# Performance work log

Measured on AMD Instinct MI355X. Metric: run time of the kernel, lower is better.

The kernel has to match this reference:

```python
import jax, jax.numpy as jnp
import numpy as np

TOP_K = 2

def setup_inputs() -> dict:
    key = jax.random.key(0)
    ks = jax.random.split(key, 8)
    B, T, C, E, I, S = 1, 2048, 2048, 8, 1408, 2816
    s = 0.02  # weight scale for numerical stability
    return {
        "x": jax.random.normal(ks[0], (B, T, C), jnp.float32),
        "gate_w": jax.random.normal(ks[1], (E, C), jnp.float32) * s,
        "w1": jax.random.normal(ks[2], (E, I, C), jnp.float32) * s,
        "w3": jax.random.normal(ks[3], (E, I, C), jnp.float32) * s,
        "w2": jax.random.normal(ks[4], (E, C, I), jnp.float32) * s,
        "sw1": jax.random.normal(ks[5], (S, C), jnp.float32) * s,
        "sw3": jax.random.normal(ks[6], (S, C), jnp.float32) * s,
        "sw2": jax.random.normal(ks[7], (C, S), jnp.float32) * s,
    }

def reference(x, gate_w, w1, w3, w2, sw1, sw3, sw2):
    B, T, C = x.shape
    E = gate_w.shape[0]
    xf = x.reshape(-1, C)                      # [N, C]
    N = xf.shape[0]
    # --- routing: top-k of raw logits, softmax over the k selected logits ---
    logits = xf @ gate_w.T                     # [N, E]
    pv, idx = jax.lax.top_k(logits, TOP_K)     # [N, K]
    pv = jax.nn.softmax(pv.astype(jnp.float32), axis=-1).astype(x.dtype)
    # token-expert combine weights (sum of probs per expert, scatter of top-k)
    tew = jnp.zeros((N, E), x.dtype).at[jnp.arange(N)[:, None], idx].add(pv)
    # --- experts (SwiGLU), computed densely over all experts and masked by tew ---
    h = jax.nn.silu(jnp.einsum('nc,eic->nei', xf, w1)) * jnp.einsum('nc,eic->nei', xf, w3)
    eo = jnp.einsum('nei,eci->nec', h, w2)     # [N, E, C]
    y = jnp.einsum('nec,ne->nc', eo, tew).reshape(B, T, C)
    # --- shared expert on the residual input ---
    sh = (jax.nn.silu(x @ sw1.T) * (x @ sw3.T)) @ sw2.T
    return y + sh
```

## Files before the change

kernel.cpp:

```cpp
#include <hip/hip_runtime.h>

#define DEVI __device__ __forceinline__

typedef __attribute__((ext_vector_type(4))) float f32x4;
typedef __attribute__((ext_vector_type(8))) short bf16x8;

static constexpr int NT = 2048;
static constexpr int CD = 2048;
static constexpr int NE = 8;
static constexpr int ID = 1408;
static constexpr int SD = 2816;
static constexpr int ROWS = 2 * NT;
static constexpr int ROWS_PAD = ROWS + 256;

DEVI unsigned short f2bf(float f) {
  unsigned u = __builtin_bit_cast(unsigned, f);
  u += 0x7fff + ((u >> 16) & 1);
  return (unsigned short)(u >> 16);
}
DEVI float bf2f(unsigned short s) { return __builtin_bit_cast(float, (unsigned)s << 16); }
DEVI float silu_f(float z) { return z / (1.f + __expf(-z)); }

DEVI void gll16(const void* g, void* l) {
  __builtin_amdgcn_global_load_lds((__attribute__((address_space(1))) void*)(void*)g,
                                   (__attribute__((address_space(3))) void*)l, 16, 0, 0);
}

DEVI void bar_sched() {
  __builtin_amdgcn_s_barrier();
  __builtin_amdgcn_sched_barrier(0);
}
DEVI void sched0() { __builtin_amdgcn_sched_barrier(0); }
DEVI void wait_vm0() { asm volatile("s_waitcnt vmcnt(0)" ::: "memory"); }
DEVI void wait_lgk0() { asm volatile("s_waitcnt lgkmcnt(0)" ::: "memory"); }

DEVI int swz8(int bid, int nwg) {
  constexpr int CH = 8, G = 64;
  int nfull = nwg - (nwg % G);
  if (bid >= nfull) return bid;
  int c = bid / G, r = bid % G;
  return c * G + (r % 8) * CH + (r / 8);
}

__global__ __launch_bounds__(256) void k_cvt(const float* __restrict__ s,
                                             unsigned short* __restrict__ d, int n8)
{
  int i = blockIdx.x * 256 + threadIdx.x;
  int stride = gridDim.x * 256;
  for (; i < n8; i += stride) {
    float4 a = ((const float4*)s)[2 * i];
    float4 b = ((const float4*)s)[2 * i + 1];
    ushort4 p0 = make_ushort4(f2bf(a.x), f2bf(a.y), f2bf(a.z), f2bf(a.w));
    ushort4 p1 = make_ushort4(f2bf(b.x), f2bf(b.y), f2bf(b.z), f2bf(b.w));
    ((ushort4*)d)[2 * i]     = p0;
    ((ushort4*)d)[2 * i + 1] = p1;
  }
}

__global__ __launch_bounds__(64) void k_router(const float* __restrict__ x,
    const float* __restrict__ gw, int* __restrict__ counts,
    int* __restrict__ eidx, int* __restrict__ posn, float* __restrict__ probs)
{
  const int n = blockIdx.x;
  const int lane = threadIdx.x;
  const float4* xr = (const float4*)(x + (size_t)n * CD);
  float acc[NE];
#pragma unroll
  for (int e = 0; e < NE; ++e) acc[e] = 0.f;
  for (int i = lane; i < CD / 4; i += 64) {
    float4 xv = xr[i];
#pragma unroll
    for (int e = 0; e < NE; ++e) {
      float4 gv = ((const float4*)(gw + (size_t)e * CD))[i];
      acc[e] += xv.x * gv.x + xv.y * gv.y + xv.z * gv.z + xv.w * gv.w;
    }
  }
#pragma unroll
  for (int e = 0; e < NE; ++e) {
    float v = acc[e];
#pragma unroll
    for (int off = 32; off > 0; off >>= 1) v += __shfl_down(v, off);
    acc[e] = v;
  }
  if (lane == 0) {
    int b0 = 0; float m0 = acc[0];
#pragma unroll
    for (int e = 1; e < NE; ++e) if (acc[e] > m0) { m0 = acc[e]; b0 = e; }
    int b1 = -1; float m1 = 0.f;
#pragma unroll
    for (int e = 0; e < NE; ++e) {
      if (e == b0) continue;
      if (b1 < 0 || acc[e] > m1) { m1 = acc[e]; b1 = e; }
    }
    float d = __expf(m1 - m0);
    float inv = 1.f / (1.f + d);
    eidx[2 * n] = b0; eidx[2 * n + 1] = b1;
    probs[2 * n] = inv; probs[2 * n + 1] = d * inv;
    posn[2 * n] = atomicAdd(&counts[b0], 1);
    posn[2 * n + 1] = atomicAdd(&counts[b1], 1);
  }
}

__global__ void k_scan(const int* __restrict__ counts, int* __restrict__ bases) {
  if (threadIdx.x == 0) {
    int s = 0;
    for (int e = 0; e < NE; ++e) { bases[e] = s; s += counts[e]; }
  }
}

__global__ __launch_bounds__(256) void k_build(const int* __restrict__ eidx,
    const int* __restrict__ posn, const int* __restrict__ bases,
    int* __restrict__ rows_of, int* __restrict__ row2tok)
{
  int n = blockIdx.x * 256 + threadIdx.x;
  if (n >= NT) return;
#pragma unroll
  for (int k = 0; k < 2; ++k) {
    int e = eidx[2 * n + k];
    int row = bases[e] + posn[2 * n + k];
    rows_of[2 * n + k] = row;
    row2tok[row] = n;
  }
}

__global__ __launch_bounds__(512, 2) void k_up(
    const unsigned short* __restrict__ xb,
    const unsigned short* __restrict__ w1b, const unsigned short* __restrict__ w3b,
    const unsigned short* __restrict__ sw1b, const unsigned short* __restrict__ sw3b,
    unsigned short* __restrict__ h, unsigned short* __restrict__ hs,
    const int* __restrict__ counts, const int* __restrict__ bases,
    const int* __restrict__ row2tok)
{
  extern __shared__ char sm[];
  constexpr int NSH = (NT / 256) * (SD / 128);
  constexpr int NWG = NSH + NE * (ID / 128) * (NT / 256);
  constexpr int NSTEP = CD / 64;

  int lin = swz8((int)blockIdx.x, NWG);
  int cls, mx, pn, e = 0;
  if (lin < NSH) { cls = 0; mx = lin % 8; pn = lin / 8; }
  else { cls = 1; int r = lin - NSH; mx = r % 8; r /= 8; pn = r % 11; e = r / 11; }

  int M = NT, baserow = 0;
  if (cls) { M = counts[e]; if (mx * 256 >= M) return; baserow = bases[e]; }
  const int m0 = mx * 256, n0 = pn * 128;

  const unsigned short* B1 = cls ? w1b + ((size_t)e * ID + n0) * CD : sw1b + (size_t)n0 * CD;
  const unsigned short* B3 = cls ? w3b + ((size_t)e * ID + n0) * CD : sw3b + (size_t)n0 * CD;

  const int tid = threadIdx.x, l = tid & 63, w = tid >> 6;
  const int wr = w >> 2, wn = w & 3;
  const int slot = ((tid & 7) ^ ((tid >> 3) & 7)) * 16;

  const char* aP[4];
#pragma unroll
  for (int t = 0; t < 4; ++t) {
    int r = t * 64 + (tid >> 3);
    const unsigned short* rb;
    if (cls) {
      int grow = m0 + r; int gr = grow < M ? grow : 0;
      rb = xb + (size_t)row2tok[baserow + gr] * CD;
    } else {
      rb = xb + (size_t)(m0 + r) * CD;
    }
    aP[t] = (const char*)rb + slot;
  }
  const char* bP1[2]; const char* bP3[2];
#pragma unroll
  for (int t = 0; t < 2; ++t) {
    int r = t * 64 + (tid >> 3);
    bP1[t] = (const char*)(B1 + (size_t)r * CD) + slot;
    bP3[t] = (const char*)(B3 + (size_t)r * CD) + slot;
  }

  f32x4 acc1[8][2], acc3[8][2];
#pragma unroll
  for (int m = 0; m < 8; ++m)
#pragma unroll
    for (int n = 0; n < 2; ++n) {
      acc1[m][n] = {0.f, 0.f, 0.f, 0.f};
      acc3[m][n] = {0.f, 0.f, 0.f, 0.f};
    }

  const int lrow = l & 15, lkg = l >> 4, l7 = l & 7;

  auto stage_first = [&](char* base, size_t kb) {
#pragma unroll
    for (int t = 0; t < 4; ++t) gll16(aP[t] + kb, base + t * 8192 + tid * 16);
  };
  auto stage_second = [&](char* base, size_t kb) {
    char* sB1 = base + 32768; char* sB3 = base + 49152;
#pragma unroll
    for (int t = 0; t < 2; ++t) {
      gll16(bP1[t] + kb, sB1 + t * 8192 + tid * 16);
      gll16(bP3[t] + kb, sB3 + t * 8192 + tid * 16);
    }
  };
  auto ldq = [&](bf16x8* fa, bf16x8* fb1, bf16x8* fb3, const char* cur, int mh, int kk) {
    const char* sA = cur; const char* sB1 = cur + 32768; const char* sB3 = cur + 49152;
    const int ao = ((kk * 4 + lkg) ^ l7) * 16;
#pragma unroll
    for (int m = 0; m < 4; ++m)
      fa[m] = *(const bf16x8*)(sA + (wr * 128 + mh * 64 + m * 16 + lrow) * 128 + ao);
#pragma unroll
    for (int n = 0; n < 2; ++n) {
      fb1[n] = *(const bf16x8*)(sB1 + (wn * 32 + n * 16 + lrow) * 128 + ao);
      fb3[n] = *(const bf16x8*)(sB3 + (wn * 32 + n * 16 + lrow) * 128 + ao);
    }
  };
  auto mmq = [&](const bf16x8* fa, const bf16x8* fb1, const bf16x8* fb3, int mh) {
    __builtin_amdgcn_s_setprio(1);
#pragma unroll
    for (int n = 0; n < 2; ++n)
#pragma unroll
      for (int m = 0; m < 4; ++m) {
        acc1[mh * 4 + m][n] = __builtin_amdgcn_mfma_f32_16x16x32_bf16(fa[m], fb1[n], acc1[mh * 4 + m][n], 0, 0, 0);
        acc3[mh * 4 + m][n] = __builtin_amdgcn_mfma_f32_16x16x32_bf16(fa[m], fb3[n], acc3[mh * 4 + m][n], 0, 0, 0);
      }
    __builtin_amdgcn_s_setprio(0);
  };

  stage_first(sm, 0);
  stage_second(sm, 0);
  wait_vm0(); bar_sched();

  bf16x8 Xa[4], Xb1[2], Xb3[2], Ya[4], Yb1[2], Yb3[2];

  for (int t = 0; t < NSTEP; ++t) {
    char* cur = sm + (size_t)(t & 1) * 65536;
    char* nxt = sm + (size_t)((t + 1) & 1) * 65536;
    size_t kb = (size_t)(t + 1) * 128;
    ldq(Xa, Xb1, Xb3, cur, 0, 0);
    sched0();
    if (t + 1 < NSTEP) stage_first(nxt, kb);
    ldq(Ya, Yb1, Yb3, cur, 1, 0);
    mmq(Xa, Xb1, Xb3, 0);
    sched0();
    if (t + 1 < NSTEP) stage_second(nxt, kb);
    ldq(Xa, Xb1, Xb3, cur, 0, 1);
    mmq(Ya, Yb1, Yb3, 1);
    sched0();
    ldq(Ya, Yb1, Yb3, cur, 1, 1);
    mmq(Xa, Xb1, Xb3, 0);
    sched0();
    mmq(Ya, Yb1, Yb3, 1);
    sched0();
    wait_vm0(); wait_lgk0();
    bar_sched();
  }

#pragma unroll
  for (int m = 0; m < 8; ++m) {
    int rb_ = m0 + wr * 128 + m * 16 + lkg * 4;
#pragma unroll
    for (int j = 0; j < 4; ++j) {
      int grow = rb_ + j;
      if (cls && grow >= M) continue;
#pragma unroll
      for (int n = 0; n < 2; ++n) {
        int gcol = n0 + wn * 32 + n * 16 + lrow;
        float hh = silu_f(acc1[m][n][j]) * acc3[m][n][j];
        if (cls) h[(size_t)(baserow + grow) * ID + gcol] = f2bf(hh);
        else     hs[(size_t)grow * SD + gcol] = f2bf(hh);
      }
    }
  }
}

__global__ __launch_bounds__(512, 2) void k_down(
    const unsigned short* __restrict__ h, const unsigned short* __restrict__ hs,
    const unsigned short* __restrict__ w2b, const unsigned short* __restrict__ sw2b,
    unsigned short* __restrict__ eo, float* __restrict__ y,
    const int* __restrict__ counts, const int* __restrict__ bases)
{
  extern __shared__ char sm[];
  constexpr int NRT = NE * (CD / 256) * (NT / 256);
  constexpr int NWG = NRT + (CD / 256) * (NT / 256);

  int lin = swz8((int)blockIdx.x, NWG);
  int cls, mx, pn, e = 0;
  if (lin < NRT) { cls = 1; mx = lin % 8; int r = lin / 8; pn = r % 8; e = r / 8; }
  else { cls = 0; int r = lin - NRT; mx = r % 8; pn = r / 8; }

  int M = NT, baserow = 0;
  if (cls) { M = counts[e]; if (mx * 256 >= M) return; baserow = bases[e]; }
  const int m0 = mx * 256, n0 = pn * 256;
  const int KD_ = cls ? ID : SD;
  const int nstep = KD_ / 64;

  const unsigned short* B = cls ? w2b + ((size_t)e * CD + n0) * ID : sw2b + (size_t)n0 * SD;

  const int tid = threadIdx.x, l = tid & 63, w = tid >> 6;
  const int wr = w >> 2, wn = w & 3;
  const int slot = ((tid & 7) ^ ((tid >> 3) & 7)) * 16;

  const char* aP[4]; const char* bP[4];
#pragma unroll
  for (int t = 0; t < 4; ++t) {
    int r = t * 64 + (tid >> 3);
    const unsigned short* rb = cls ? h + (size_t)(baserow + m0 + r) * ID
                                   : hs + (size_t)(m0 + r) * SD;
    aP[t] = (const char*)rb + slot;
    bP[t] = (const char*)(B + (size_t)r * KD_) + slot;
  }

  f32x4 acc[8][4];
#pragma unroll
  for (int m = 0; m < 8; ++m)
#pragma unroll
    for (int n = 0; n < 4; ++n) acc[m][n] = {0.f, 0.f, 0.f, 0.f};

  const int lrow = l & 15, lkg = l >> 4, l7 = l & 7;

  auto stage_first = [&](char* base, size_t kb) {
#pragma unroll
    for (int t = 0; t < 4; ++t) gll16(aP[t] + kb, base + t * 8192 + tid * 16);
  };
  auto stage_second = [&](char* base, size_t kb) {
    char* sB = base + 32768;
#pragma unroll
    for (int t = 0; t < 4; ++t) gll16(bP[t] + kb, sB + t * 8192 + tid * 16);
  };
  auto ldq = [&](bf16x8* fa, bf16x8* fb, const char* cur, int mh, int kk) {
    const char* sA = cur; const char* sB = cur + 32768;
    const int ao = ((kk * 4 + lkg) ^ l7) * 16;
#pragma unroll
    for (int m = 0; m < 4; ++m)
      fa[m] = *(const bf16x8*)(sA + (wr * 128 + mh * 64 + m * 16 + lrow) * 128 + ao);
#pragma unroll
    for (int n = 0; n < 4; ++n)
      fb[n] = *(const bf16x8*)(sB + (wn * 64 + n * 16 + lrow) * 128 + ao);
  };
  auto mmq = [&](const bf16x8* fa, const bf16x8* fb, int mh) {
    __builtin_amdgcn_s_setprio(1);
#pragma unroll
    for (int n = 0; n < 4; ++n)
#pragma unroll
      for (int m = 0; m < 4; ++m)
        acc[mh * 4 + m][n] = __builtin_amdgcn_mfma_f32_16x16x32_bf16(fa[m], fb[n], acc[mh * 4 + m][n], 0, 0, 0);
    __builtin_amdgcn_s_setprio(0);
  };

  stage_first(sm, 0);
  stage_second(sm, 0);
  wait_vm0(); bar_sched();

  bf16x8 Xa[4], Xb[4], Ya[4], Yb[4];

  for (int t = 0; t < nstep; ++t) {
    char* cur = sm + (size_t)(t & 1) * 65536;
    char* nxt = sm + (size_t)((t + 1) & 1) * 65536;
    size_t kb = (size_t)(t + 1) * 128;
    ldq(Xa, Xb, cur, 0, 0);
    sched0();
    if (t + 1 < nstep) stage_first(nxt, kb);
    ldq(Ya, Yb, cur, 1, 0);
    mmq(Xa, Xb, 0);
    sched0();
    if (t + 1 < nstep) stage_second(nxt, kb);
    ldq(Xa, Xb, cur, 0, 1);
    mmq(Ya, Yb, 1);
    sched0();
    ldq(Ya, Yb, cur, 1, 1);
    mmq(Xa, Xb, 0);
    sched0();
    mmq(Ya, Yb, 1);
    sched0();
    wait_vm0(); wait_lgk0();
    bar_sched();
  }

#pragma unroll
  for (int m = 0; m < 8; ++m) {
    int rb_ = m0 + wr * 128 + m * 16 + lkg * 4;
#pragma unroll
    for (int j = 0; j < 4; ++j) {
      int grow = rb_ + j;
      if (cls && grow >= M) continue;
#pragma unroll
      for (int n = 0; n < 4; ++n) {
        int gcol = n0 + wn * 64 + n * 16 + lrow;
        float v = acc[m][n][j];
        if (cls) eo[(size_t)(baserow + grow) * CD + gcol] = f2bf(v);
        else     y[(size_t)grow * CD + gcol] = v;
      }
    }
  }
}

__global__ __launch_bounds__(256) void k_combine(float* __restrict__ y,
    const unsigned short* __restrict__ eo, const int* __restrict__ rows_of,
    const float* __restrict__ probs)
{
  const int n = blockIdx.x;
  const int c = threadIdx.x * 8;
  const int r0 = rows_of[2 * n], r1 = rows_of[2 * n + 1];
  const float p0 = probs[2 * n], p1 = probs[2 * n + 1];
  bf16x8 e0 = *(const bf16x8*)(eo + (size_t)r0 * CD + c);
  bf16x8 e1 = *(const bf16x8*)(eo + (size_t)r1 * CD + c);
  float* yp = y + (size_t)n * CD + c;
  float4 y0 = *(float4*)yp, y1 = *(float4*)(yp + 4);
  y0.x += p0 * bf2f((unsigned short)e0[0]) + p1 * bf2f((unsigned short)e1[0]);
  y0.y += p0 * bf2f((unsigned short)e0[1]) + p1 * bf2f((unsigned short)e1[1]);
  y0.z += p0 * bf2f((unsigned short)e0[2]) + p1 * bf2f((unsigned short)e1[2]);
  y0.w += p0 * bf2f((unsigned short)e0[3]) + p1 * bf2f((unsigned short)e1[3]);
  y1.x += p0 * bf2f((unsigned short)e0[4]) + p1 * bf2f((unsigned short)e1[4]);
  y1.y += p0 * bf2f((unsigned short)e0[5]) + p1 * bf2f((unsigned short)e1[5]);
  y1.z += p0 * bf2f((unsigned short)e0[6]) + p1 * bf2f((unsigned short)e1[6]);
  y1.w += p0 * bf2f((unsigned short)e0[7]) + p1 * bf2f((unsigned short)e1[7]);
  *(float4*)yp = y0; *(float4*)(yp + 4) = y1;
}

extern "C" void kernel_launch(void* const* d_in, const int* in_sizes, int n_in,
                              void* d_out, int out_size, void* d_ws, size_t ws_size,
                              hipStream_t stream)
{
  const float* x   = (const float*)d_in[0];
  const float* gw  = (const float*)d_in[1];
  const float* w1  = (const float*)d_in[2];
  const float* w3  = (const float*)d_in[3];
  const float* w2  = (const float*)d_in[4];
  const float* sw1 = (const float*)d_in[5];
  const float* sw3 = (const float*)d_in[6];
  const float* sw2 = (const float*)d_in[7];
  float* y = (float*)d_out;

  char* p = (char*)d_ws;
  auto alloc = [&](size_t b) { char* r = p; p += (b + 255) & ~(size_t)255; return r; };
  int*   counts  = (int*)alloc(NE * 4);
  int*   bases   = (int*)alloc(NE * 4);
  int*   eidx    = (int*)alloc((size_t)NT * 2 * 4);
  int*   posn    = (int*)alloc((size_t)NT * 2 * 4);
  float* probs   = (float*)alloc((size_t)NT * 2 * 4);
  int*   rows_of = (int*)alloc((size_t)NT * 2 * 4);
  int*   row2tok = (int*)alloc((size_t)ROWS * 4);
  unsigned short* xb   = (unsigned short*)alloc((size_t)NT * CD * 2);
  unsigned short* w1b  = (unsigned short*)alloc((size_t)NE * ID * CD * 2);
  unsigned short* w3b  = (unsigned short*)alloc((size_t)NE * ID * CD * 2);
  unsigned short* w2b  = (unsigned short*)alloc((size_t)NE * CD * ID * 2);
  unsigned short* sw1b = (unsigned short*)alloc((size_t)SD * CD * 2);
  unsigned short* sw3b = (unsigned short*)alloc((size_t)SD * CD * 2);
  unsigned short* sw2b = (unsigned short*)alloc((size_t)CD * SD * 2);
  unsigned short* h    = (unsigned short*)alloc((size_t)ROWS_PAD * ID * 2);
  unsigned short* eo   = (unsigned short*)alloc((size_t)ROWS_PAD * CD * 2);
  unsigned short* hs   = (unsigned short*)alloc((size_t)NT * SD * 2);

  hipFuncSetAttribute((const void*)k_up,   hipFuncAttributeMaxDynamicSharedMemorySize, 131072);
  hipFuncSetAttribute((const void*)k_down, hipFuncAttributeMaxDynamicSharedMemorySize, 131072);

  hipMemsetAsync(counts, 0, NE * 4, stream);

  auto cvt = [&](const float* s, unsigned short* d, size_t n) {
    int n8 = (int)(n / 8);
    int grid = (n8 + 255) / 256; if (grid > 2048) grid = 2048;
    k_cvt<<<grid, 256, 0, stream>>>(s, d, n8);
  };
  cvt(x,   xb,   (size_t)NT * CD);
  cvt(w1,  w1b,  (size_t)NE * ID * CD);
  cvt(w3,  w3b,  (size_t)NE * ID * CD);
  cvt(w2,  w2b,  (size_t)NE * CD * ID);
  cvt(sw1, sw1b, (size_t)SD * CD);
  cvt(sw3, sw3b, (size_t)SD * CD);
  cvt(sw2, sw2b, (size_t)CD * SD);

  k_router<<<NT, 64, 0, stream>>>(x, gw, counts, eidx, posn, probs);
  k_scan<<<1, 64, 0, stream>>>(counts, bases);
  k_build<<<NT / 256, 256, 0, stream>>>(eidx, posn, bases, rows_of, row2tok);

  {
    constexpr int NWG = (NT / 256) * (SD / 128) + NE * (ID / 128) * (NT / 256);
    k_up<<<NWG, 512, 131072, stream>>>(xb, w1b, w3b, sw1b, sw3b, h, hs,
                                       counts, bases, row2tok);
  }
  {
    constexpr int NWG = NE * (CD / 256) * (NT / 256) + (CD / 256) * (NT / 256);
    k_down<<<NWG, 512, 131072, stream>>>(h, hs, w2b, sw2b, eo, y, counts, bases);
  }
  k_combine<<<NT, 256, 0, stream>>>(y, eo, rows_of, probs);
}
```

Measured before the change: 437.1 us.

## Split down-projection into templated 128x128 GEMMs and fuse combine into shared GEMM

Replaces the single 256x256-tile k_down kernel (routed and shared experts in one grid) with a templated 128x128-tile, 256-thread GEMM launched twice: once for routed experts writing eo, then once for the shared expert. The shared-expert epilogue reads the two routed rows for each token and adds their prob-weighted values, so the separate k_combine kernel and its y read-modify-write are gone. The pipeline now uses static 64KB LDS with double buffering and vmcnt(8) partial waits, plus a new chunked block swizzle. Smaller tiles mean more launched blocks and less data reuse per block. The shared GEMM can no longer overlap with the routed GEMM, and its epilogue does scattered bf16 gathers from eo.

```diff
diff --git a/kernel.cpp b/kernel.cpp
--- a/kernel.cpp
+++ b/kernel.cpp
@@ -31,11 +31,19 @@
   __builtin_amdgcn_sched_barrier(0);
 }
 DEVI void sched0() { __builtin_amdgcn_sched_barrier(0); }
+DEVI void wait_vm8() { asm volatile("s_waitcnt vmcnt(8)" ::: "memory"); }
 DEVI void wait_vm0() { asm volatile("s_waitcnt vmcnt(0)" ::: "memory"); }
 DEVI void wait_lgk0() { asm volatile("s_waitcnt lgkmcnt(0)" ::: "memory"); }
 
 DEVI int swz8(int bid, int nwg) {
   constexpr int CH = 8, G = 64;
+  int nfull = nwg - (nwg % G);
+  if (bid >= nfull) return bid;
+  int c = bid / G, r = bid % G;
+  return c * G + (r % 8) * CH + (r / 8);
+}
+DEVI int swz_chunk(int bid, int nwg) {
+  constexpr int CH = 16, G = 8 * CH;
   int nfull = nwg - (nwg % G);
   if (bid >= nfull) return bid;
   int c = bid / G, r = bid % G;
@@ -267,148 +275,149 @@
   }
 }
 
-__global__ __launch_bounds__(512, 2) void k_down(
-    const unsigned short* __restrict__ h, const unsigned short* __restrict__ hs,
-    const unsigned short* __restrict__ w2b, const unsigned short* __restrict__ sw2b,
-    unsigned short* __restrict__ eo, float* __restrict__ y,
-    const int* __restrict__ counts, const int* __restrict__ bases)
-{
-  extern __shared__ char sm[];
-  constexpr int NRT = NE * (CD / 256) * (NT / 256);
-  constexpr int NWG = NRT + (CD / 256) * (NT / 256);
-
-  int lin = swz8((int)blockIdx.x, NWG);
-  int cls, mx, pn, e = 0;
-  if (lin < NRT) { cls = 1; mx = lin % 8; int r = lin / 8; pn = r % 8; e = r / 8; }
-  else { cls = 0; int r = lin - NRT; mx = r % 8; pn = r / 8; }
-
-  int M = NT, baserow = 0;
-  if (cls) { M = counts[e]; if (mx * 256 >= M) return; baserow = bases[e]; }
-  const int m0 = mx * 256, n0 = pn * 256;
-  const int KD_ = cls ? ID : SD;
-  const int nstep = KD_ / 64;
-
-  const unsigned short* B = cls ? w2b + ((size_t)e * CD + n0) * ID : sw2b + (size_t)n0 * SD;
+struct GArgs {
+  const unsigned short* A;
+  const unsigned short* B1;
+  void* Out;
+  const int* counts; const int* bases;
+  const int* rows_of; const float* probs; const unsigned short* eo;
+};
+
+template<int MODE>
+__global__ __launch_bounds__(256) void k_gemm(GArgs a)
+{
+  constexpr int KD = (MODE == 1 ? ID : SD);
+  constexpr int BN = 128;
+  constexpr int NH = BN / 2;
+  constexpr int NFT = NH / 16;
+  constexpr int BT = 4;
+  constexpr int NMB = NT / 128;
+  constexpr int NPN = CD / 128;
+  constexpr int NWG = NMB * NPN * ((MODE == 1) ? NE : 1);
+  constexpr int NSTEP = KD / 64;
+
+  __shared__ __align__(16) char smem[2][32768];
+
+  int lin = swz_chunk((int)blockIdx.x, NWG);
+  const int mx = lin % NMB; lin /= NMB;
+  const int pn = lin % NPN;
+  const int e  = lin / NPN;
+
+  int M, baserow = 0;
+  if constexpr (MODE == 1) {
+    int ne = a.counts[e];
+    if (mx * 128 >= ne) return;
+    M = ne; baserow = a.bases[e];
+  } else { M = NT; }
+  const int m0 = mx * 128;
+  const int n0 = pn * BN;
+
+  const unsigned short* B1;
+  if constexpr (MODE == 1) { B1 = a.B1 + ((size_t)e * CD + n0) * ID; }
+  else                     { B1 = a.B1 + (size_t)n0 * SD; }
 
   const int tid = threadIdx.x, l = tid & 63, w = tid >> 6;
-  const int wr = w >> 2, wn = w & 3;
-  const int slot = ((tid & 7) ^ ((tid >> 3) & 7)) * 16;
-
-  const char* aP[4]; const char* bP[4];
+  const int wr = w >> 1, wc = w & 1;
+  const int slot = ((l & 7) ^ ((l >> 3) & 7)) * 16;
+
+  const char* aP[4];
 #pragma unroll
   for (int t = 0; t < 4; ++t) {
-    int r = t * 64 + (tid >> 3);
-    const unsigned short* rb = cls ? h + (size_t)(baserow + m0 + r) * ID
-                                   : hs + (size_t)(m0 + r) * SD;
+    int r = w * 32 + t * 8 + (l >> 3);
+    const unsigned short* rb;
+    if constexpr (MODE == 1) {
+      rb = a.A + (size_t)(baserow + m0 + r) * KD;
+    } else {
+      rb = a.A + (size_t)(m0 + r) * KD;
+    }
     aP[t] = (const char*)rb + slot;
-    bP[t] = (const char*)(B + (size_t)r * KD_) + slot;
-  }
-
-  f32x4 acc[8][4];
-#pragma unroll
-  for (int m = 0; m < 8; ++m)
-#pragma unroll
-    for (int n = 0; n < 4; ++n) acc[m][n] = {0.f, 0.f, 0.f, 0.f};
+  }
+  const char* bP1[BT];
+#pragma unroll
+  for (int t = 0; t < BT; ++t) {
+    int r = w * (8 * BT) + t * 8 + (l >> 3);
+    bP1[t] = (const char*)(B1 + (size_t)r * KD) + slot;
+  }
+
+  f32x4 acc1[4][NFT];
+#pragma unroll
+  for (int m = 0; m < 4; ++m)
+#pragma unroll
+    for (int n = 0; n < NFT; ++n) acc1[m][n] = {0.f, 0.f, 0.f, 0.f};
 
   const int lrow = l & 15, lkg = l >> 4, l7 = l & 7;
-
-  auto stage_first = [&](char* base, size_t kb) {
-#pragma unroll
-    for (int t = 0; t < 4; ++t) gll16(aP[t] + kb, base + t * 8192 + tid * 16);
-  };
-  auto stage_second = [&](char* base, size_t kb) {
-    char* sB = base + 32768;
-#pragma unroll
-    for (int t = 0; t < 4; ++t) gll16(bP[t] + kb, sB + t * 8192 + tid * 16);
-  };
-  auto ldq = [&](bf16x8* fa, bf16x8* fb, const char* cur, int mh, int kk) {
-    const char* sA = cur; const char* sB = cur + 32768;
-    const int ao = ((kk * 4 + lkg) ^ l7) * 16;
-#pragma unroll
-    for (int m = 0; m < 4; ++m)
-      fa[m] = *(const bf16x8*)(sA + (wr * 128 + mh * 64 + m * 16 + lrow) * 128 + ao);
-#pragma unroll
-    for (int n = 0; n < 4; ++n)
-      fb[n] = *(const bf16x8*)(sB + (wn * 64 + n * 16 + lrow) * 128 + ao);
-  };
-  auto mmq = [&](const bf16x8* fa, const bf16x8* fb, int mh) {
-    __builtin_amdgcn_s_setprio(1);
-#pragma unroll
-    for (int n = 0; n < 4; ++n)
+  const int ao0 = (lkg ^ l7) * 16;
+  const int ao1 = ((4 + lkg) ^ l7) * 16;
+
+  auto stageF = [&](char* base, size_t kb) {
+    char* sA = base; char* sB1 = base + 16384;
+#pragma unroll
+    for (int t = 0; t < 4; ++t) gll16(aP[t] + kb, sA + (w * 4 + t) * 1024);
+#pragma unroll
+    for (int t = 0; t < BT; ++t) gll16(bP1[t] + kb, sB1 + (w * BT + t) * 1024);
+  };
+  auto computeF = [&](const char* base) {
+    const char* sA = base; const char* sB1 = base + 16384;
+#pragma unroll
+    for (int kk = 0; kk < 2; ++kk) {
+      const int ao = kk ? ao1 : ao0;
+      bf16x8 af[4];
 #pragma unroll
       for (int m = 0; m < 4; ++m)
-        acc[mh * 4 + m][n] = __builtin_amdgcn_mfma_f32_16x16x32_bf16(fa[m], fb[n], acc[mh * 4 + m][n], 0, 0, 0);
-    __builtin_amdgcn_s_setprio(0);
-  };
-
-  stage_first(sm, 0);
-  stage_second(sm, 0);
+        af[m] = *(const bf16x8*)(sA + (wr * 64 + m * 16 + lrow) * 128 + ao);
+#pragma unroll
+      for (int n = 0; n < NFT; ++n) {
+        bf16x8 b1 = *(const bf16x8*)(sB1 + (wc * NH + n * 16 + lrow) * 128 + ao);
+#pragma unroll
+        for (int m = 0; m < 4; ++m)
+          acc1[m][n] = __builtin_amdgcn_mfma_f32_16x16x32_bf16(af[m], b1, acc1[m][n], 0, 0, 0);
+      }
+    }
+  };
+
+  stageF(smem[0], 0);
+  int t = 0;
+  for (; t < NSTEP - 2; t += 2) {
+    stageF(smem[1], (size_t)(t + 1) * 128);
+    wait_vm8(); bar_sched();
+    computeF(smem[0]);
+    wait_lgk0(); bar_sched();
+    stageF(smem[0], (size_t)(t + 2) * 128);
+    wait_vm8(); bar_sched();
+    computeF(smem[1]);
+    wait_lgk0(); bar_sched();
+  }
+  stageF(smem[1], (size_t)(NSTEP - 1) * 128);
+  wait_vm8(); bar_sched();
+  computeF(smem[0]);
   wait_vm0(); bar_sched();
-
-  bf16x8 Xa[4], Xb[4], Ya[4], Yb[4];
-
-  for (int t = 0; t < nstep; ++t) {
-    char* cur = sm + (size_t)(t & 1) * 65536;
-    char* nxt = sm + (size_t)((t + 1) & 1) * 65536;
-    size_t kb = (size_t)(t + 1) * 128;
-    ldq(Xa, Xb, cur, 0, 0);
-    sched0();
-    if (t + 1 < nstep) stage_first(nxt, kb);
-    ldq(Ya, Yb, cur, 1, 0);
-    mmq(Xa, Xb, 0);
-    sched0();
-    if (t + 1 < nstep) stage_second(nxt, kb);
-    ldq(Xa, Xb, cur, 0, 1);
-    mmq(Ya, Yb, 1);
-    sched0();
-    ldq(Ya, Yb, cur, 1, 1);
-    mmq(Xa, Xb, 0);
-    sched0();
-    mmq(Ya, Yb, 1);
-    sched0();
-    wait_vm0(); wait_lgk0();
-    bar_sched();
-  }
-
-#pragma unroll
-  for (int m = 0; m < 8; ++m) {
-    int rb_ = m0 + wr * 128 + m * 16 + lkg * 4;
+  computeF(smem[1]);
+
+#pragma unroll
+  for (int m = 0; m < 4; ++m) {
+    int rbase = m0 + wr * 64 + m * 16 + lkg * 4;
 #pragma unroll
     for (int j = 0; j < 4; ++j) {
-      int grow = rb_ + j;
-      if (cls && grow >= M) continue;
-#pragma unroll
-      for (int n = 0; n < 4; ++n) {
-        int gcol = n0 + wn * 64 + n * 16 + lrow;
-        float v = acc[m][n][j];
-        if (cls) eo[(size_t)(baserow + grow) * CD + gcol] = f2bf(v);
-        else     y[(size_t)grow * CD + gcol] = v;
+      int grow = rbase + j;
+      if constexpr (MODE == 1) { if (grow >= M) continue; }
+      int r0 = 0, r1 = 0; float p0 = 0.f, p1 = 0.f;
+      if constexpr (MODE == 3) {
+        r0 = a.rows_of[2 * grow]; r1 = a.rows_of[2 * grow + 1];
+        p0 = a.probs[2 * grow];   p1 = a.probs[2 * grow + 1];
       }
-    }
-  }
-}
-
-__global__ __launch_bounds__(256) void k_combine(float* __restrict__ y,
-    const unsigned short* __restrict__ eo, const int* __restrict__ rows_of,
-    const float* __restrict__ probs)
-{
-  const int n = blockIdx.x;
-  const int c = threadIdx.x * 8;
-  const int r0 = rows_of[2 * n], r1 = rows_of[2 * n + 1];
-  const float p0 = probs[2 * n], p1 = probs[2 * n + 1];
-  bf16x8 e0 = *(const bf16x8*)(eo + (size_t)r0 * CD + c);
-  bf16x8 e1 = *(const bf16x8*)(eo + (size_t)r1 * CD + c);
-  float* yp = y + (size_t)n * CD + c;
-  float4 y0 = *(float4*)yp, y1 = *(float4*)(yp + 4);
-  y0.x += p0 * bf2f((unsigned short)e0[0]) + p1 * bf2f((unsigned short)e1[0]);
-  y0.y += p0 * bf2f((unsigned short)e0[1]) + p1 * bf2f((unsigned short)e1[1]);
-  y0.z += p0 * bf2f((unsigned short)e0[2]) + p1 * bf2f((unsigned short)e1[2]);
-  y0.w += p0 * bf2f((unsigned short)e0[3]) + p1 * bf2f((unsigned short)e1[3]);
-  y1.x += p0 * bf2f((unsigned short)e0[4]) + p1 * bf2f((unsigned short)e1[4]);
-  y1.y += p0 * bf2f((unsigned short)e0[5]) + p1 * bf2f((unsigned short)e1[5]);
-  y1.z += p0 * bf2f((unsigned short)e0[6]) + p1 * bf2f((unsigned short)e1[6]);
-  y1.w += p0 * bf2f((unsigned short)e0[7]) + p1 * bf2f((unsigned short)e1[7]);
-  *(float4*)yp = y0; *(float4*)(yp + 4) = y1;
+#pragma unroll
+      for (int n = 0; n < NFT; ++n) {
+        int gcol = n0 + wc * NH + n * 16 + lrow;
+        float v1 = acc1[m][n][j];
+        if constexpr (MODE == 1) {
+          ((unsigned short*)a.Out)[(size_t)(baserow + grow) * CD + gcol] = f2bf(v1);
+        } else {
+          float vv = v1 + p0 * bf2f(a.eo[(size_t)r0 * CD + gcol]) + p1 * bf2f(a.eo[(size_t)r1 * CD + gcol]);
+          ((float*)a.Out)[(size_t)grow * CD + gcol] = vv;
+        }
+      }
+    }
+  }
 }
 
 extern "C" void kernel_launch(void* const* d_in, const int* in_sizes, int n_in,
@@ -445,8 +454,7 @@
   unsigned short* eo   = (unsigned short*)alloc((size_t)ROWS_PAD * CD * 2);
   unsigned short* hs   = (unsigned short*)alloc((size_t)NT * SD * 2);
 
-  hipFuncSetAttribute((const void*)k_up,   hipFuncAttributeMaxDynamicSharedMemorySize, 131072);
-  hipFuncSetAttribute((const void*)k_down, hipFuncAttributeMaxDynamicSharedMemorySize, 131072);
+  hipFuncSetAttribute((const void*)k_up, hipFuncAttributeMaxDynamicSharedMemorySize, 131072);
 
   hipMemsetAsync(counts, 0, NE * 4, stream);
 
@@ -473,8 +481,13 @@
                                        counts, bases, row2tok);
   }
   {
-    constexpr int NWG = NE * (CD / 256) * (NT / 256) + (CD / 256) * (NT / 256);
-    k_down<<<NWG, 512, 131072, stream>>>(h, hs, w2b, sw2b, eo, y, counts, bases);
-  }
-  k_combine<<<NT, 256, 0, stream>>>(y, eo, rows_of, probs);
-}
+    GArgs g{}; g.A = h; g.B1 = w2b; g.Out = eo;
+    g.counts = counts; g.bases = bases;
+    k_gemm<1><<<(NT / 128) * (CD / 128) * NE, 256, 0, stream>>>(g);
+  }
+  {
+    GArgs g{}; g.A = hs; g.B1 = sw2b; g.Out = y;
+    g.rows_of = rows_of; g.probs = probs; g.eo = eo;
+    k_gemm<3><<<(NT / 128) * (CD / 128), 256, 0, stream>>>(g);
+  }
+}
```

New measurement: 411.4 us. -5.9%, faster.
